# Kernel optimization log

Hardware: AMD Instinct MI355X
Metric: run time of the kernel (lower is better)

Reference implementation:

```python
import jax, jax.numpy as jnp
import numpy as np
import itertools

GRID = 256          # voxel grid extent per axis (coords in [0, GRID))
KSIZE = 3           # kernel_size
OFFSETS = np.array(list(itertools.product(range(KSIZE), repeat=3)), dtype=np.int32) - (KSIZE // 2)  # [27,3]


def setup_inputs() -> dict:
    key = jax.random.key(0)
    k1, k2, k3 = jax.random.split(key, 3)
    N, Cin, Cout = 262144, 64, 64
    coords = jax.random.randint(k1, (N, 3), 0, GRID, dtype=jnp.int32)
    feats = jax.random.normal(k2, (N, Cin), dtype=jnp.float32)
    kernel = jax.random.normal(k3, (KSIZE ** 3, Cin, Cout), dtype=jnp.float32) * 0.02
    return {"coords": coords, "feats": feats, "kernel": kernel}


def reference(coords, feats, kernel):
    # Submanifold sparse conv3d: out[i] = sum_k feats[j_k(i)] @ kernel[k]
    # where coords[j_k(i)] == coords[i] + offset_k (if such a point exists).
    N = coords.shape[0]
    Cout = kernel.shape[-1]
    # Hash table: linearized voxel -> point index (-1 if empty).
    lin = (coords[:, 0] * GRID + coords[:, 1]) * GRID + coords[:, 2]
    table = jnp.full((GRID ** 3,), -1, dtype=jnp.int32).at[lin].set(
        jnp.arange(N, dtype=jnp.int32))
    out = jnp.zeros((N, Cout), dtype=feats.dtype)
    for k in range(KSIZE ** 3):
        off = jnp.asarray(OFFSETS[k])              # [3]
        nc = coords + off[None, :]                 # neighbor coords [N,3]
        in_bounds = jnp.all((nc >= 0) & (nc < GRID), axis=1)
        nlin = (nc[:, 0] * GRID + nc[:, 1]) * GRID + nc[:, 2]
        idx = table[jnp.clip(nlin, 0, GRID ** 3 - 1)]
        valid = in_bounds & (idx >= 0)
        g = feats[jnp.where(valid, idx, 0)] * valid[:, None].astype(feats.dtype)  # [N,Cin]
        out = out + g @ kernel[k]                  # [N,Cout]
    return out
```

## Files before the change

kernel.cpp:

```cpp
#include <hip/hip_runtime.h>

#define VGRID 256
#define N_TAPS 27
#define CIN 64
#define COUT 64
#define BPTS 64
#define HBITS 20
#define HSIZE (1u << HBITS)
#define HEMPTY 0xFFFFFFFFFFFFFFFFull

typedef short short8 __attribute__((ext_vector_type(8)));
typedef float float4v __attribute__((ext_vector_type(4)));

__device__ __forceinline__ short f2bf(float x) {
    unsigned u = __builtin_bit_cast(unsigned, x);
    unsigned r = (u + 0x7FFF + ((u >> 16) & 1)) >> 16;
    return (short)r;
}

__device__ __forceinline__ unsigned hslot(int lin) {
    return ((unsigned)lin * 2654435761u) >> (32 - HBITS);
}

__device__ __forceinline__ int hlookup(const unsigned long long* __restrict__ hash,
                                       int lin) {
    unsigned s = hslot(lin);
    for (;;) {
        unsigned long long e = hash[s];
        if ((unsigned)(e >> 32) == (unsigned)lin) return (int)(unsigned)e;
        s = (s + 1) & (HSIZE - 1);
    }
}

__global__ void __launch_bounds__(256) build_kernel(
        const int* __restrict__ coords, unsigned long long* __restrict__ hash,
        unsigned* __restrict__ bits, const float* __restrict__ W,
        short* __restrict__ Wt, const float* __restrict__ F,
        short* __restrict__ Fb, int n, int bt_blocks, int fb_elems) {
    int b = (int)blockIdx.x;
    if (b >= bt_blocks + N_TAPS) {
        int idx = (b - bt_blocks - N_TAPS) * 256 + (int)threadIdx.x;
        int e = idx * 8;
        if (e < fb_elems) {
            const float4v* s = (const float4v*)(F + e);
            float4v x = __builtin_nontemporal_load(s);
            float4v y = __builtin_nontemporal_load(s + 1);
            short8 o = {f2bf(x[0]), f2bf(x[1]), f2bf(x[2]), f2bf(x[3]),
                        f2bf(y[0]), f2bf(y[1]), f2bf(y[2]), f2bf(y[3])};
            *(short8*)(Fb + e) = o;
        }
        return;
    }
    if (b >= bt_blocks) {
        int tap = b - bt_blocks;
        for (int e = threadIdx.x; e < CIN * COUT; e += 256) {
            int ci = e >> 6, co = e & 63;
            int ks = ci >> 5, quad = (ci >> 3) & 3, el = ci & 7;
            Wt[((((size_t)tap * 2 + ks) * 4 + quad) * 64 + co) * 8 + el] =
                f2bf(W[((size_t)tap * CIN + ci) * COUT + co]);
        }
        return;
    }
    int i = b * 256 + threadIdx.x;
    if (i >= n) return;
    int lin = (coords[i * 3 + 0] * VGRID + coords[i * 3 + 1]) * VGRID + coords[i * 3 + 2];
    unsigned long long want = ((unsigned long long)(unsigned)lin << 32) | (unsigned)i;
    unsigned s = hslot(lin);
    for (;;) {
        unsigned long long old = atomicCAS(&hash[s], HEMPTY, want);
        if (old == HEMPTY) break;
        if ((unsigned)(old >> 32) == (unsigned)lin) { atomicMax(&hash[s], want); break; }
        s = (s + 1) & (HSIZE - 1);
    }
    atomicOr(&bits[lin >> 5], 1u << (lin & 31));
}

__global__ void __launch_bounds__(256) fused_kernel(
        const int* __restrict__ coords, const unsigned long long* __restrict__ hash,
        const unsigned* __restrict__ bits, const short* __restrict__ featsb,
        const short* __restrict__ Wt, float* __restrict__ out, int n) {
    __shared__ int s_pk[BPTS];
    __shared__ unsigned s_hm[4][BPTS];
    __shared__ int s_jc[BPTS];
    __shared__ int s_p[4][BPTS];

    int t = threadIdx.x;
    int p = t & (BPTS - 1);
    int q = t >> 6;
    int i = blockIdx.x * BPTS + p;

    int cx = 0, cy = 0, cz = 0;
    unsigned pmask = 0;
    if (i < n) {
        cx = coords[i * 3 + 0];
        cy = coords[i * 3 + 1];
        cz = coords[i * 3 + 2];
        if (q == 0) s_jc[p] = hlookup(hash, (cx * VGRID + cy) * VGRID + cz);

        int zlo = cz > 0 ? cz - 1 : 0;
        int zhi = cz < VGRID - 1 ? cz + 1 : VGRID - 1;
        int wlo = zlo >> 5, whi = zhi >> 5;
        int nr = (q == 3) ? 3 : 2;
        int r0 = 2 * q;
        unsigned rwa[3], rwb[3];
#pragma unroll
        for (int rr = 0; rr < 3; ++rr) {
            int r = r0 + rr;
            int nx = cx + r / 3 - 1, ny = cy + r % 3 - 1;
            bool v = (rr < nr) && ((unsigned)nx < VGRID) && ((unsigned)ny < VGRID);
            int rb = ((nx * VGRID + ny) * VGRID) >> 5;
            rwa[rr] = v ? bits[rb + wlo] : 0u;
            rwb[rr] = v ? bits[rb + whi] : 0u;
        }
#pragma unroll
        for (int rr = 0; rr < 3; ++rr) {
            int r = r0 + rr;
#pragma unroll
            for (int zz = 0; zz < 3; ++zz) {
                int k = r * 3 + zz;
                int nz = cz + zz - 1;
                if (rr < nr && k != 13 && (unsigned)nz < VGRID) {
                    unsigned wrd = ((nz >> 5) == wlo) ? rwa[rr] : rwb[rr];
                    pmask |= ((wrd >> (nz & 31)) & 1u) << k;
                }
            }
        }
    }
    if (q == 0) {
        s_pk[p] = (cx << 16) | (cy << 8) | cz;
        if (i >= n) s_jc[p] = 0;
    }
    s_hm[q][p] = pmask;
    __syncthreads();

    {
        unsigned hmc = s_hm[0][p] | s_hm[1][p] | s_hm[2][p] | s_hm[3][p];
        if (q == 0) s_hm[0][p] = hmc;
        unsigned mm = hmc;
#pragma unroll
        for (int d = 0; d < 3; ++d) if (d < q) mm &= mm - 1u;
        int ja = 0;
        if (mm) {
            int kA = __builtin_ctz(mm);
            ja = hlookup(hash, ((cx + kA / 9 - 1) * VGRID + (cy + (kA / 3) % 3 - 1))
                               * VGRID + (cz + kA % 3 - 1));
        }
        s_p[q][p] = ja;
    }
    __syncthreads();

    int lane = t & 63;
    int m = lane & 15, quad = lane >> 4;
    const short8* Bp = (const short8*)Wt;
    const short8* Fp = (const short8*)featsb;
    int base = blockIdx.x * BPTS;

    int row = q * 16 + m;
    unsigned rhm = s_hm[0][row];
    int rjc = s_jc[row];

    unsigned gor = rhm;
    gor |= (unsigned)__shfl_xor((int)gor, 1);
    gor |= (unsigned)__shfl_xor((int)gor, 2);
    gor |= (unsigned)__shfl_xor((int)gor, 4);
    gor |= (unsigned)__shfl_xor((int)gor, 8);
    gor = __builtin_amdgcn_readfirstlane(gor);

    float4v acc[4] = {{0,0,0,0},{0,0,0,0},{0,0,0,0},{0,0,0,0}};

    {
        short8 a0 = Fp[(size_t)rjc * 8 + quad];
        short8 a1 = Fp[(size_t)rjc * 8 + 4 + quad];
#pragma unroll
        for (int nt = 0; nt < 4; ++nt) {
            short8 b0 = Bp[((13 * 2 + 0) * 4 + quad) * 64 + nt * 16 + m];
            short8 b1 = Bp[((13 * 2 + 1) * 4 + quad) * 64 + nt * 16 + m];
            acc[nt] = __builtin_amdgcn_mfma_f32_16x16x32_bf16(a0, b0, acc[nt], 0, 0, 0);
            acc[nt] = __builtin_amdgcn_mfma_f32_16x16x32_bf16(a1, b1, acc[nt], 0, 0, 0);
        }
    }

    unsigned gm = gor;
    while (gm) {
        int k = (int)__builtin_ctz(gm); gm &= gm - 1u;
        bool has = (rhm >> k) & 1u;
        short8 h0 = {0,0,0,0,0,0,0,0}, h1 = {0,0,0,0,0,0,0,0};
        if (has) {
            int rank = __builtin_popcount(rhm & ((1u << k) - 1u));
            int j2;
            if (rank < 4) {
                j2 = s_p[rank][row];
            } else {
                int rpk = s_pk[row];
                int rx = (rpk >> 16) & 255, ry = (rpk >> 8) & 255, rz = rpk & 255;
                j2 = hlookup(hash, ((rx + k / 9 - 1) * VGRID + (ry + (k / 3) % 3 - 1))
                                   * VGRID + (rz + k % 3 - 1));
            }
            h0 = Fp[(size_t)j2 * 8 + quad];
            h1 = Fp[(size_t)j2 * 8 + 4 + quad];
        }
#pragma unroll
        for (int nt = 0; nt < 4; ++nt) {
            short8 b0 = Bp[((k * 2 + 0) * 4 + quad) * 64 + nt * 16 + m];
            short8 b1 = Bp[((k * 2 + 1) * 4 + quad) * 64 + nt * 16 + m];
            acc[nt] = __builtin_amdgcn_mfma_f32_16x16x32_bf16(h0, b0, acc[nt], 0, 0, 0);
            acc[nt] = __builtin_amdgcn_mfma_f32_16x16x32_bf16(h1, b1, acc[nt], 0, 0, 0);
        }
    }

#pragma unroll
    for (int nt = 0; nt < 4; ++nt)
#pragma unroll
        for (int r2 = 0; r2 < 4; ++r2) {
            int orow = base + q * 16 + quad * 4 + r2;
            if (orow < n) out[(size_t)orow * COUT + nt * 16 + m] = acc[nt][r2];
        }
}

extern "C" void kernel_launch(void* const* d_in, const int* in_sizes, int n_in,
                              void* d_out, int out_size, void* d_ws, size_t ws_size,
                              hipStream_t stream) {
    const int* coords = (const int*)d_in[0];
    const float* feats = (const float*)d_in[1];
    const float* weights = (const float*)d_in[2];
    float* out = (float*)d_out;

    int n = in_sizes[0] / 3;

    char* ws = (char*)d_ws;
    size_t BITMAP_BYTES = (size_t)VGRID * VGRID * VGRID / 8;
    unsigned* bits = (unsigned*)ws;
    unsigned long long* hash = (unsigned long long*)(ws + BITMAP_BYTES);
    short* wbft = (short*)(ws + ((size_t)10 << 20));
    short* fb = (short*)(ws + ((size_t)11 << 20));

    hipMemsetAsync(ws, 0, BITMAP_BYTES, stream);
    hipMemsetAsync(ws + BITMAP_BYTES, 0xFF, (size_t)HSIZE * 8, stream);

    int bt_blocks = (n + 255) / 256;
    int fb_elems = n * CIN;
    int conv_blocks = (fb_elems / 8 + 255) / 256;
    build_kernel<<<bt_blocks + N_TAPS + conv_blocks, 256, 0, stream>>>(
        coords, hash, bits, weights, wbft, feats, fb, n, bt_blocks, fb_elems);

    int f_blocks = (n + BPTS - 1) / BPTS;
    fused_kernel<<<f_blocks, 256, 0, stream>>>(coords, hash, bits, fb, wbft, out, n);
}
```

Measured before the change: 207.4 us.

## Process two point tiles per block and overlap next tile's lookups with GEMM

The fused kernel now handles two 64-point tiles per block. The second tile's coordinate, bitmap and hash loads are issued before the first tile's neighbor combine and GEMM, so their latency can hide behind that work. The build kernel is split into a scatter kernel and a convert kernel, and the convert kernel now does 16 elements per thread with nontemporal stores. Costs are double the shared memory, more live registers, half as many blocks, and an extra kernel launch.

```diff
diff --git a/kernel.cpp b/kernel.cpp
--- a/kernel.cpp
+++ b/kernel.cpp
@@ -22,9 +22,8 @@
     return ((unsigned)lin * 2654435761u) >> (32 - HBITS);
 }
 
-__device__ __forceinline__ int hlookup(const unsigned long long* __restrict__ hash,
-                                       int lin) {
-    unsigned s = hslot(lin);
+__device__ __forceinline__ int hwalk(const unsigned long long* __restrict__ hash,
+                                     int lin, unsigned s) {
     for (;;) {
         unsigned long long e = hash[s];
         if ((unsigned)(e >> 32) == (unsigned)lin) return (int)(unsigned)e;
@@ -32,36 +31,15 @@
     }
 }
 
-__global__ void __launch_bounds__(256) build_kernel(
+__device__ __forceinline__ int hlookup(const unsigned long long* __restrict__ hash,
+                                       int lin) {
+    return hwalk(hash, lin, hslot(lin));
+}
+
+__global__ void __launch_bounds__(256) build_scatter(
         const int* __restrict__ coords, unsigned long long* __restrict__ hash,
-        unsigned* __restrict__ bits, const float* __restrict__ W,
-        short* __restrict__ Wt, const float* __restrict__ F,
-        short* __restrict__ Fb, int n, int bt_blocks, int fb_elems) {
-    int b = (int)blockIdx.x;
-    if (b >= bt_blocks + N_TAPS) {
-        int idx = (b - bt_blocks - N_TAPS) * 256 + (int)threadIdx.x;
-        int e = idx * 8;
-        if (e < fb_elems) {
-            const float4v* s = (const float4v*)(F + e);
-            float4v x = __builtin_nontemporal_load(s);
-            float4v y = __builtin_nontemporal_load(s + 1);
-            short8 o = {f2bf(x[0]), f2bf(x[1]), f2bf(x[2]), f2bf(x[3]),
-                        f2bf(y[0]), f2bf(y[1]), f2bf(y[2]), f2bf(y[3])};
-            *(short8*)(Fb + e) = o;
-        }
-        return;
-    }
-    if (b >= bt_blocks) {
-        int tap = b - bt_blocks;
-        for (int e = threadIdx.x; e < CIN * COUT; e += 256) {
-            int ci = e >> 6, co = e & 63;
-            int ks = ci >> 5, quad = (ci >> 3) & 3, el = ci & 7;
-            Wt[((((size_t)tap * 2 + ks) * 4 + quad) * 64 + co) * 8 + el] =
-                f2bf(W[((size_t)tap * CIN + ci) * COUT + co]);
-        }
-        return;
-    }
-    int i = b * 256 + threadIdx.x;
+        unsigned* __restrict__ bits, int n) {
+    int i = blockIdx.x * 256 + threadIdx.x;
     if (i >= n) return;
     int lin = (coords[i * 3 + 0] * VGRID + coords[i * 3 + 1]) * VGRID + coords[i * 3 + 2];
     unsigned long long want = ((unsigned long long)(unsigned)lin << 32) | (unsigned)i;
@@ -75,67 +53,125 @@
     atomicOr(&bits[lin >> 5], 1u << (lin & 31));
 }
 
+__global__ void __launch_bounds__(256) build_convert(
+        const float* __restrict__ W, short* __restrict__ Wt,
+        const float* __restrict__ F, short* __restrict__ Fb, int fb_elems) {
+    int b = (int)blockIdx.x;
+    if (b < N_TAPS) {
+        int tap = b;
+        for (int e = threadIdx.x; e < CIN * COUT; e += 256) {
+            int ci = e >> 6, co = e & 63;
+            int ks = ci >> 5, quad = (ci >> 3) & 3, el = ci & 7;
+            Wt[((((size_t)tap * 2 + ks) * 4 + quad) * 64 + co) * 8 + el] =
+                f2bf(W[((size_t)tap * CIN + ci) * COUT + co]);
+        }
+        return;
+    }
+    int idx = (b - N_TAPS) * 256 + (int)threadIdx.x;
+    int e = idx * 16;
+    if (e < fb_elems) {
+        const float4v* s = (const float4v*)(F + e);
+        float4v x0 = __builtin_nontemporal_load(s);
+        float4v x1 = __builtin_nontemporal_load(s + 1);
+        float4v x2 = __builtin_nontemporal_load(s + 2);
+        float4v x3 = __builtin_nontemporal_load(s + 3);
+        short8 o0 = {f2bf(x0[0]), f2bf(x0[1]), f2bf(x0[2]), f2bf(x0[3]),
+                     f2bf(x1[0]), f2bf(x1[1]), f2bf(x1[2]), f2bf(x1[3])};
+        short8 o1 = {f2bf(x2[0]), f2bf(x2[1]), f2bf(x2[2]), f2bf(x2[3]),
+                     f2bf(x3[0]), f2bf(x3[1]), f2bf(x3[2]), f2bf(x3[3])};
+        __builtin_nontemporal_store(o0, (short8*)(Fb + e));
+        __builtin_nontemporal_store(o1, (short8*)(Fb + e + 8));
+    }
+}
+
 __global__ void __launch_bounds__(256) fused_kernel(
         const int* __restrict__ coords, const unsigned long long* __restrict__ hash,
         const unsigned* __restrict__ bits, const short* __restrict__ featsb,
         const short* __restrict__ Wt, float* __restrict__ out, int n) {
-    __shared__ int s_pk[BPTS];
-    __shared__ unsigned s_hm[4][BPTS];
-    __shared__ int s_jc[BPTS];
-    __shared__ int s_p[4][BPTS];
+    __shared__ int s_pk[2][BPTS];
+    __shared__ unsigned s_hm[2][4][BPTS];
+    __shared__ int s_jc[2][BPTS];
+    __shared__ int s_p[2][4][BPTS];
 
     int t = threadIdx.x;
     int p = t & (BPTS - 1);
     int q = t >> 6;
-    int i = blockIdx.x * BPTS + p;
-
-    int cx = 0, cy = 0, cz = 0;
-    unsigned pmask = 0;
-    if (i < n) {
-        cx = coords[i * 3 + 0];
-        cy = coords[i * 3 + 1];
-        cz = coords[i * 3 + 2];
-        if (q == 0) s_jc[p] = hlookup(hash, (cx * VGRID + cy) * VGRID + cz);
-
-        int zlo = cz > 0 ? cz - 1 : 0;
-        int zhi = cz < VGRID - 1 ? cz + 1 : VGRID - 1;
-        int wlo = zlo >> 5, whi = zhi >> 5;
-        int nr = (q == 3) ? 3 : 2;
-        int r0 = 2 * q;
-        unsigned rwa[3], rwb[3];
-#pragma unroll
-        for (int rr = 0; rr < 3; ++rr) {
-            int r = r0 + rr;
-            int nx = cx + r / 3 - 1, ny = cy + r % 3 - 1;
-            bool v = (rr < nr) && ((unsigned)nx < VGRID) && ((unsigned)ny < VGRID);
-            int rb = ((nx * VGRID + ny) * VGRID) >> 5;
-            rwa[rr] = v ? bits[rb + wlo] : 0u;
-            rwb[rr] = v ? bits[rb + whi] : 0u;
-        }
-#pragma unroll
-        for (int rr = 0; rr < 3; ++rr) {
-            int r = r0 + rr;
-#pragma unroll
-            for (int zz = 0; zz < 3; ++zz) {
-                int k = r * 3 + zz;
-                int nz = cz + zz - 1;
-                if (rr < nr && k != 13 && (unsigned)nz < VGRID) {
-                    unsigned wrd = ((nz >> 5) == wlo) ? rwa[rr] : rwb[rr];
-                    pmask |= ((wrd >> (nz & 31)) & 1u) << k;
+    int lane = t & 63;
+    int m = lane & 15, quad = lane >> 4;
+    const short8* Bp = (const short8*)Wt;
+    const short8* Fp = (const short8*)featsb;
+
+    auto issue = [&](int i, int& cx, int& cy, int& cz,
+                     unsigned (&wa)[3], unsigned (&wb)[3],
+                     unsigned long long& e0, unsigned& s0) {
+        cx = 0; cy = 0; cz = 0; e0 = 0; s0 = 0;
+#pragma unroll
+        for (int rr = 0; rr < 3; ++rr) { wa[rr] = 0u; wb[rr] = 0u; }
+        if (i < n) {
+            cx = coords[i * 3 + 0];
+            cy = coords[i * 3 + 1];
+            cz = coords[i * 3 + 2];
+            if (q == 0) {
+                s0 = hslot((cx * VGRID + cy) * VGRID + cz);
+                e0 = hash[s0];
+            }
+            int zlo = cz > 0 ? cz - 1 : 0;
+            int zhi = cz < VGRID - 1 ? cz + 1 : VGRID - 1;
+            int wlo = zlo >> 5, whi = zhi >> 5;
+            int nr = (q == 3) ? 3 : 2;
+            int r0 = 2 * q;
+#pragma unroll
+            for (int rr = 0; rr < 3; ++rr) {
+                int r = r0 + rr;
+                int nx = cx + r / 3 - 1, ny = cy + r % 3 - 1;
+                bool v = (rr < nr) && ((unsigned)nx < VGRID) && ((unsigned)ny < VGRID);
+                int rb = ((nx * VGRID + ny) * VGRID) >> 5;
+                wa[rr] = v ? bits[rb + wlo] : 0u;
+                wb[rr] = v ? bits[rb + whi] : 0u;
+            }
+        }
+    };
+
+    auto finish = [&](int c, int i, int cx, int cy, int cz,
+                      unsigned (&wa)[3], unsigned (&wb)[3],
+                      unsigned long long e0, unsigned s0) {
+        unsigned pmask = 0;
+        if (i < n) {
+            int zlo = cz > 0 ? cz - 1 : 0;
+            int wlo = zlo >> 5;
+            int nr = (q == 3) ? 3 : 2;
+            int r0 = 2 * q;
+#pragma unroll
+            for (int rr = 0; rr < 3; ++rr) {
+                int r = r0 + rr;
+#pragma unroll
+                for (int zz = 0; zz < 3; ++zz) {
+                    int k = r * 3 + zz;
+                    int nz = cz + zz - 1;
+                    if (rr < nr && k != 13 && (unsigned)nz < VGRID) {
+                        unsigned wrd = ((nz >> 5) == wlo) ? wa[rr] : wb[rr];
+                        pmask |= ((wrd >> (nz & 31)) & 1u) << k;
+                    }
                 }
             }
         }
-    }
-    if (q == 0) {
-        s_pk[p] = (cx << 16) | (cy << 8) | cz;
-        if (i >= n) s_jc[p] = 0;
-    }
-    s_hm[q][p] = pmask;
-    __syncthreads();
-
-    {
-        unsigned hmc = s_hm[0][p] | s_hm[1][p] | s_hm[2][p] | s_hm[3][p];
-        if (q == 0) s_hm[0][p] = hmc;
+        s_hm[c][q][p] = pmask;
+        if (q == 0) {
+            s_pk[c][p] = (cx << 16) | (cy << 8) | cz;
+            int jc = 0;
+            if (i < n) {
+                int lin = (cx * VGRID + cy) * VGRID + cz;
+                jc = ((unsigned)(e0 >> 32) == (unsigned)lin)
+                         ? (int)(unsigned)e0
+                         : hwalk(hash, lin, (s0 + 1) & (HSIZE - 1));
+            }
+            s_jc[c][p] = jc;
+        }
+    };
+
+    auto combine = [&](int c, int cx, int cy, int cz) {
+        unsigned hmc = s_hm[c][0][p] | s_hm[c][1][p] | s_hm[c][2][p] | s_hm[c][3][p];
+        if (q == 0) s_hm[c][0][p] = hmc;
         unsigned mm = hmc;
 #pragma unroll
         for (int d = 0; d < 3; ++d) if (d < q) mm &= mm - 1u;
@@ -145,76 +181,96 @@
             ja = hlookup(hash, ((cx + kA / 9 - 1) * VGRID + (cy + (kA / 3) % 3 - 1))
                                * VGRID + (cz + kA % 3 - 1));
         }
-        s_p[q][p] = ja;
-    }
+        s_p[c][q][p] = ja;
+    };
+
+    auto gemm = [&](int c, int base) {
+        int row = q * 16 + m;
+        unsigned rhm = s_hm[c][0][row];
+        int rjc = s_jc[c][row];
+
+        unsigned gor = rhm;
+        gor |= (unsigned)__shfl_xor((int)gor, 1);
+        gor |= (unsigned)__shfl_xor((int)gor, 2);
+        gor |= (unsigned)__shfl_xor((int)gor, 4);
+        gor |= (unsigned)__shfl_xor((int)gor, 8);
+        gor = __builtin_amdgcn_readfirstlane(gor);
+
+        float4v acc[4] = {{0,0,0,0},{0,0,0,0},{0,0,0,0},{0,0,0,0}};
+
+        {
+            short8 a0 = Fp[(size_t)rjc * 8 + quad];
+            short8 a1 = Fp[(size_t)rjc * 8 + 4 + quad];
+#pragma unroll
+            for (int nt = 0; nt < 4; ++nt) {
+                short8 b0 = Bp[((13 * 2 + 0) * 4 + quad) * 64 + nt * 16 + m];
+                short8 b1 = Bp[((13 * 2 + 1) * 4 + quad) * 64 + nt * 16 + m];
+                acc[nt] = __builtin_amdgcn_mfma_f32_16x16x32_bf16(a0, b0, acc[nt], 0, 0, 0);
+                acc[nt] = __builtin_amdgcn_mfma_f32_16x16x32_bf16(a1, b1, acc[nt], 0, 0, 0);
+            }
+        }
+
+        unsigned gm = gor;
+        while (gm) {
+            int k = (int)__builtin_ctz(gm); gm &= gm - 1u;
+            bool has = (rhm >> k) & 1u;
+            short8 h0 = {0,0,0,0,0,0,0,0}, h1 = {0,0,0,0,0,0,0,0};
+            if (has) {
+                int rank = __builtin_popcount(rhm & ((1u << k) - 1u));
+                int j2;
+                if (rank < 4) {
+                    j2 = s_p[c][rank][row];
+                } else {
+                    int rpk = s_pk[c][row];
+                    int rx = (rpk >> 16) & 255, ry = (rpk >> 8) & 255, rz = rpk & 255;
+                    j2 = hlookup(hash, ((rx + k / 9 - 1) * VGRID + (ry + (k / 3) % 3 - 1))
+                                       * VGRID + (rz + k % 3 - 1));
+                }
+                h0 = Fp[(size_t)j2 * 8 + quad];
+                h1 = Fp[(size_t)j2 * 8 + 4 + quad];
+            }
+#pragma unroll
+            for (int nt = 0; nt < 4; ++nt) {
+                short8 b0 = Bp[((k * 2 + 0) * 4 + quad) * 64 + nt * 16 + m];
+                short8 b1 = Bp[((k * 2 + 1) * 4 + quad) * 64 + nt * 16 + m];
+                acc[nt] = __builtin_amdgcn_mfma_f32_16x16x32_bf16(h0, b0, acc[nt], 0, 0, 0);
+                acc[nt] = __builtin_amdgcn_mfma_f32_16x16x32_bf16(h1, b1, acc[nt], 0, 0, 0);
+            }
+        }
+
+#pragma unroll
+        for (int nt = 0; nt < 4; ++nt)
+#pragma unroll
+            for (int r2 = 0; r2 < 4; ++r2) {
+                int orow = base + q * 16 + quad * 4 + r2;
+                if (orow < n) out[(size_t)orow * COUT + nt * 16 + m] = acc[nt][r2];
+            }
+    };
+
+    int base0 = blockIdx.x * BPTS;
+    int base1 = (blockIdx.x + gridDim.x) * BPTS;
+    int i0 = base0 + p;
+    int i1 = base1 + p;
+
+    int cx0, cy0, cz0; unsigned wa0[3], wb0[3]; unsigned long long e0; unsigned sl0;
+    issue(i0, cx0, cy0, cz0, wa0, wb0, e0, sl0);
+    finish(0, i0, cx0, cy0, cz0, wa0, wb0, e0, sl0);
     __syncthreads();
 
-    int lane = t & 63;
-    int m = lane & 15, quad = lane >> 4;
-    const short8* Bp = (const short8*)Wt;
-    const short8* Fp = (const short8*)featsb;
-    int base = blockIdx.x * BPTS;
-
-    int row = q * 16 + m;
-    unsigned rhm = s_hm[0][row];
-    int rjc = s_jc[row];
-
-    unsigned gor = rhm;
-    gor |= (unsigned)__shfl_xor((int)gor, 1);
-    gor |= (unsigned)__shfl_xor((int)gor, 2);
-    gor |= (unsigned)__shfl_xor((int)gor, 4);
-    gor |= (unsigned)__shfl_xor((int)gor, 8);
-    gor = __builtin_amdgcn_readfirstlane(gor);
-
-    float4v acc[4] = {{0,0,0,0},{0,0,0,0},{0,0,0,0},{0,0,0,0}};
-
-    {
-        short8 a0 = Fp[(size_t)rjc * 8 + quad];
-        short8 a1 = Fp[(size_t)rjc * 8 + 4 + quad];
-#pragma unroll
-        for (int nt = 0; nt < 4; ++nt) {
-            short8 b0 = Bp[((13 * 2 + 0) * 4 + quad) * 64 + nt * 16 + m];
-            short8 b1 = Bp[((13 * 2 + 1) * 4 + quad) * 64 + nt * 16 + m];
-            acc[nt] = __builtin_amdgcn_mfma_f32_16x16x32_bf16(a0, b0, acc[nt], 0, 0, 0);
-            acc[nt] = __builtin_amdgcn_mfma_f32_16x16x32_bf16(a1, b1, acc[nt], 0, 0, 0);
-        }
-    }
-
-    unsigned gm = gor;
-    while (gm) {
-        int k = (int)__builtin_ctz(gm); gm &= gm - 1u;
-        bool has = (rhm >> k) & 1u;
-        short8 h0 = {0,0,0,0,0,0,0,0}, h1 = {0,0,0,0,0,0,0,0};
-        if (has) {
-            int rank = __builtin_popcount(rhm & ((1u << k) - 1u));
-            int j2;
-            if (rank < 4) {
-                j2 = s_p[rank][row];
-            } else {
-                int rpk = s_pk[row];
-                int rx = (rpk >> 16) & 255, ry = (rpk >> 8) & 255, rz = rpk & 255;
-                j2 = hlookup(hash, ((rx + k / 9 - 1) * VGRID + (ry + (k / 3) % 3 - 1))
-                                   * VGRID + (rz + k % 3 - 1));
-            }
-            h0 = Fp[(size_t)j2 * 8 + quad];
-            h1 = Fp[(size_t)j2 * 8 + 4 + quad];
-        }
-#pragma unroll
-        for (int nt = 0; nt < 4; ++nt) {
-            short8 b0 = Bp[((k * 2 + 0) * 4 + quad) * 64 + nt * 16 + m];
-            short8 b1 = Bp[((k * 2 + 1) * 4 + quad) * 64 + nt * 16 + m];
-            acc[nt] = __builtin_amdgcn_mfma_f32_16x16x32_bf16(h0, b0, acc[nt], 0, 0, 0);
-            acc[nt] = __builtin_amdgcn_mfma_f32_16x16x32_bf16(h1, b1, acc[nt], 0, 0, 0);
-        }
-    }
-
-#pragma unroll
-    for (int nt = 0; nt < 4; ++nt)
-#pragma unroll
-        for (int r2 = 0; r2 < 4; ++r2) {
-            int orow = base + q * 16 + quad * 4 + r2;
-            if (orow < n) out[(size_t)orow * COUT + nt * 16 + m] = acc[nt][r2];
-        }
+    int cx1, cy1, cz1; unsigned wa1[3], wb1[3]; unsigned long long e1; unsigned sl1;
+    issue(i1, cx1, cy1, cz1, wa1, wb1, e1, sl1);
+
+    combine(0, cx0, cy0, cz0);
+    __syncthreads();
+
+    gemm(0, base0);
+
+    finish(1, i1, cx1, cy1, cz1, wa1, wb1, e1, sl1);
+    __syncthreads();
+    combine(1, cx1, cy1, cz1);
+    __syncthreads();
+
+    gemm(1, base1);
 }
 
 extern "C" void kernel_launch(void* const* d_in, const int* in_sizes, int n_in,
@@ -238,11 +294,13 @@
     hipMemsetAsync(ws + BITMAP_BYTES, 0xFF, (size_t)HSIZE * 8, stream);
 
     int bt_blocks = (n + 255) / 256;
+    build_scatter<<<bt_blocks, 256, 0, stream>>>(coords, hash, bits, n);
+
     int fb_elems = n * CIN;
-    int conv_blocks = (fb_elems / 8 + 255) / 256;
-    build_kernel<<<bt_blocks + N_TAPS + conv_blocks, 256, 0, stream>>>(
-        coords, hash, bits, weights, wbft, feats, fb, n, bt_blocks, fb_elems);
-
-    int f_blocks = (n + BPTS - 1) / BPTS;
+    int conv_blocks = (fb_elems / 16 + 255) / 256;
+    build_convert<<<N_TAPS + conv_blocks, 256, 0, stream>>>(
+        weights, wbft, feats, fb, fb_elems);
+
+    int f_blocks = (n + 2 * BPTS - 1) / (2 * BPTS);
     fused_kernel<<<f_blocks, 256, 0, stream>>>(coords, hash, bits, fb, wbft, out, n);
 }
```

Result: slower. 239.1 us (+15.3%).

## Software-pipeline neighbor gathers and precompute up to eight neighbor indices

Applied to the files above, without the earlier changes.

The main tap loop is restructured so the gather of the next tap's features is issued before the MFMAs for the current tap, overlapping global-load latency with matrix work. The precomputed neighbor index table in shared memory grows from four to eight ranks per point, so fewer in-loop hash lookups fall back to serial probing. The feature conversion pass now handles 16 elements per thread and uses nontemporal stores. These changes raise register pressure from the double-buffered fragments and add hash lookups to the prologue.

```diff
diff --git a/kernel.cpp b/kernel.cpp
--- a/kernel.cpp
+++ b/kernel.cpp
@@ -40,14 +40,19 @@
     int b = (int)blockIdx.x;
     if (b >= bt_blocks + N_TAPS) {
         int idx = (b - bt_blocks - N_TAPS) * 256 + (int)threadIdx.x;
-        int e = idx * 8;
+        int e = idx * 16;
         if (e < fb_elems) {
             const float4v* s = (const float4v*)(F + e);
-            float4v x = __builtin_nontemporal_load(s);
-            float4v y = __builtin_nontemporal_load(s + 1);
-            short8 o = {f2bf(x[0]), f2bf(x[1]), f2bf(x[2]), f2bf(x[3]),
-                        f2bf(y[0]), f2bf(y[1]), f2bf(y[2]), f2bf(y[3])};
-            *(short8*)(Fb + e) = o;
+            float4v x0 = __builtin_nontemporal_load(s);
+            float4v x1 = __builtin_nontemporal_load(s + 1);
+            float4v x2 = __builtin_nontemporal_load(s + 2);
+            float4v x3 = __builtin_nontemporal_load(s + 3);
+            short8 o0 = {f2bf(x0[0]), f2bf(x0[1]), f2bf(x0[2]), f2bf(x0[3]),
+                         f2bf(x1[0]), f2bf(x1[1]), f2bf(x1[2]), f2bf(x1[3])};
+            short8 o1 = {f2bf(x2[0]), f2bf(x2[1]), f2bf(x2[2]), f2bf(x2[3]),
+                         f2bf(x3[0]), f2bf(x3[1]), f2bf(x3[2]), f2bf(x3[3])};
+            __builtin_nontemporal_store(o0, (short8*)(Fb + e));
+            __builtin_nontemporal_store(o1, (short8*)(Fb + e + 8));
         }
         return;
     }
@@ -82,7 +87,7 @@
     __shared__ int s_pk[BPTS];
     __shared__ unsigned s_hm[4][BPTS];
     __shared__ int s_jc[BPTS];
-    __shared__ int s_p[4][BPTS];
+    __shared__ int s_p[8][BPTS];
 
     int t = threadIdx.x;
     int p = t & (BPTS - 1);
@@ -139,13 +144,22 @@
         unsigned mm = hmc;
 #pragma unroll
         for (int d = 0; d < 3; ++d) if (d < q) mm &= mm - 1u;
-        int ja = 0;
+        int ja = 0, jb = 0;
         if (mm) {
             int kA = __builtin_ctz(mm);
             ja = hlookup(hash, ((cx + kA / 9 - 1) * VGRID + (cy + (kA / 3) % 3 - 1))
                                * VGRID + (cz + kA % 3 - 1));
+            unsigned mm2 = mm;
+            mm2 &= mm2 - 1u; if (mm2) mm2 &= mm2 - 1u;
+            if (mm2) mm2 &= mm2 - 1u; if (mm2) mm2 &= mm2 - 1u;
+            if (mm2) {
+                int kB = __builtin_ctz(mm2);
+                jb = hlookup(hash, ((cx + kB / 9 - 1) * VGRID + (cy + (kB / 3) % 3 - 1))
+                                   * VGRID + (cz + kB % 3 - 1));
+            }
         }
         s_p[q][p] = ja;
+        s_p[q + 4][p] = jb;
     }
     __syncthreads();
 
@@ -158,6 +172,10 @@
     int row = q * 16 + m;
     unsigned rhm = s_hm[0][row];
     int rjc = s_jc[row];
+
+    int kA = 13;
+    short8 fA0 = Fp[(size_t)rjc * 8 + quad];
+    short8 fA1 = Fp[(size_t)rjc * 8 + 4 + quad];
 
     unsigned gor = rhm;
     gor |= (unsigned)__shfl_xor((int)gor, 1);
@@ -168,44 +186,36 @@
 
     float4v acc[4] = {{0,0,0,0},{0,0,0,0},{0,0,0,0},{0,0,0,0}};
 
-    {
-        short8 a0 = Fp[(size_t)rjc * 8 + quad];
-        short8 a1 = Fp[(size_t)rjc * 8 + 4 + quad];
+    unsigned gm = gor;
+    while (kA >= 0) {
+        int kB = -1;
+        short8 fB0 = {0,0,0,0,0,0,0,0}, fB1 = {0,0,0,0,0,0,0,0};
+        if (gm) {
+            kB = (int)__builtin_ctz(gm); gm &= gm - 1u;
+            if ((rhm >> kB) & 1u) {
+                int rank = __builtin_popcount(rhm & ((1u << kB) - 1u));
+                int j2;
+                if (rank < 8) {
+                    j2 = s_p[rank][row];
+                } else {
+                    int rpk = s_pk[row];
+                    int rx = (rpk >> 16) & 255, ry = (rpk >> 8) & 255, rz = rpk & 255;
+                    j2 = hlookup(hash, ((rx + kB / 9 - 1) * VGRID
+                                        + (ry + (kB / 3) % 3 - 1)) * VGRID
+                                       + (rz + kB % 3 - 1));
+                }
+                fB0 = Fp[(size_t)j2 * 8 + quad];
+                fB1 = Fp[(size_t)j2 * 8 + 4 + quad];
+            }
+        }
 #pragma unroll
         for (int nt = 0; nt < 4; ++nt) {
-            short8 b0 = Bp[((13 * 2 + 0) * 4 + quad) * 64 + nt * 16 + m];
-            short8 b1 = Bp[((13 * 2 + 1) * 4 + quad) * 64 + nt * 16 + m];
-            acc[nt] = __builtin_amdgcn_mfma_f32_16x16x32_bf16(a0, b0, acc[nt], 0, 0, 0);
-            acc[nt] = __builtin_amdgcn_mfma_f32_16x16x32_bf16(a1, b1, acc[nt], 0, 0, 0);
-        }
-    }
-
-    unsigned gm = gor;
-    while (gm) {
-        int k = (int)__builtin_ctz(gm); gm &= gm - 1u;
-        bool has = (rhm >> k) & 1u;
-        short8 h0 = {0,0,0,0,0,0,0,0}, h1 = {0,0,0,0,0,0,0,0};
-        if (has) {
-            int rank = __builtin_popcount(rhm & ((1u << k) - 1u));
-            int j2;
-            if (rank < 4) {
-                j2 = s_p[rank][row];
-            } else {
-                int rpk = s_pk[row];
-                int rx = (rpk >> 16) & 255, ry = (rpk >> 8) & 255, rz = rpk & 255;
-                j2 = hlookup(hash, ((rx + k / 9 - 1) * VGRID + (ry + (k / 3) % 3 - 1))
-                                   * VGRID + (rz + k % 3 - 1));
-            }
-            h0 = Fp[(size_t)j2 * 8 + quad];
-            h1 = Fp[(size_t)j2 * 8 + 4 + quad];
-        }
-#pragma unroll
-        for (int nt = 0; nt < 4; ++nt) {
-            short8 b0 = Bp[((k * 2 + 0) * 4 + quad) * 64 + nt * 16 + m];
-            short8 b1 = Bp[((k * 2 + 1) * 4 + quad) * 64 + nt * 16 + m];
-            acc[nt] = __builtin_amdgcn_mfma_f32_16x16x32_bf16(h0, b0, acc[nt], 0, 0, 0);
-            acc[nt] = __builtin_amdgcn_mfma_f32_16x16x32_bf16(h1, b1, acc[nt], 0, 0, 0);
-        }
+            short8 b0 = Bp[((kA * 2 + 0) * 4 + quad) * 64 + nt * 16 + m];
+            short8 b1 = Bp[((kA * 2 + 1) * 4 + quad) * 64 + nt * 16 + m];
+            acc[nt] = __builtin_amdgcn_mfma_f32_16x16x32_bf16(fA0, b0, acc[nt], 0, 0, 0);
+            acc[nt] = __builtin_amdgcn_mfma_f32_16x16x32_bf16(fA1, b1, acc[nt], 0, 0, 0);
+        }
+        kA = kB; fA0 = fB0; fA1 = fB1;
     }
 
 #pragma unroll
@@ -239,7 +249,7 @@
 
     int bt_blocks = (n + 255) / 256;
     int fb_elems = n * CIN;
-    int conv_blocks = (fb_elems / 8 + 255) / 256;
+    int conv_blocks = (fb_elems / 16 + 255) / 256;
     build_kernel<<<bt_blocks + N_TAPS + conv_blocks, 256, 0, stream>>>(
         coords, hash, bits, weights, wbft, feats, fb, n, bt_blocks, fb_elems);
 
```

Result: slower. 223.1 us (+7.6%).
